# Kernel optimization log

Hardware: AMD Instinct MI355X
Metric: run time of the kernel (lower is better)

Reference implementation:

```python
import jax, jax.numpy as jnp
import numpy as np

D_K = 64
D_V = 64


def _scan_stream(q, k, v):
    """Process one stream of L tokens; q,k: (L, d_k), v: (L, d_v).
    Faithful to the torch module: update() calls update_correlations(k, q, v),
    i.e. arguments swapped, so Sigma_qv is EMA of k outer v and Sigma_qq is EMA of k outer k.
    Returns per-token cost values, shape (L,).
    """
    d_k, d_v = q.shape[-1], v.shape[-1]

    def step(carry, qkv):
        Svv, Skv, Skk, J, l = carry
        qt, kt, vt = qkv
        l = l + 1.0
        w = 1.0 / l          # omega_i
        wf = 1.0 - w         # omega_f == (l-1)/l
        Svv = wf * Svv + w * jnp.outer(vt, vt)   # (d_v, d_v)
        Skv = wf * Skv + w * jnp.outer(kt, vt)   # (d_k, d_v)  <- 'Sigma_qv' with swapped args
        Skk = wf * Skk + w * jnp.outer(kt, kt)   # (d_k, d_k)  <- 'Sigma_qq' with swapped args
        J = wf * J + w * jnp.outer(vt, kt)       # (d_v, d_k)
        # C = 1/2 Tr(Svv) - Tr(J Skv) + 1/2 Tr(J Skk J^T)
        term1 = 0.5 * jnp.trace(Svv)
        term2 = -jnp.sum(J * Skv.T)              # Tr(J @ Skv)
        term3 = 0.5 * jnp.sum((J @ Skk) * J)     # Tr(J @ Skk @ J^T)
        return (Svv, Skv, Skk, J, l), term1 + term2 + term3

    init = (jnp.zeros((d_v, d_v), q.dtype),
            jnp.zeros((d_k, d_v), q.dtype),
            jnp.zeros((d_k, d_k), q.dtype),
            jnp.zeros((d_v, d_k), q.dtype),
            jnp.asarray(0.0, q.dtype))
    _, costs = jax.lax.scan(step, init, (q, k, v))
    return costs


def setup_inputs() -> dict:
    key = jax.random.key(0)
    kq, kk, kv = jax.random.split(key, 3)
    B, L = 8, 2048
    q = jax.random.normal(kq, (B, L, D_K), dtype=jnp.float32)
    k = jax.random.normal(kk, (B, L, D_K), dtype=jnp.float32)
    v = jax.random.normal(kv, (B, L, D_V), dtype=jnp.float32)
    return {"q": q, "k": k, "v": v}


def reference(q, k, v):
    # (B, L) per-token costs for B independent memory streams
    return jax.vmap(_scan_stream)(q, k, v)
```

## Files before the change

### kernel.cpp

```cpp
#include <hip/hip_runtime.h>

#define BB 8
#define LL 2048
#define CC 64
#define NCH 32
#define SB 72

typedef float f32x4 __attribute__((ext_vector_type(4)));
typedef short bf8 __attribute__((ext_vector_type(8)));

static __device__ __forceinline__ unsigned short f2b(float f) {
  unsigned u = __builtin_bit_cast(unsigned, f);
  u += 0x7fff + ((u >> 16) & 1);
  return (unsigned short)(u >> 16);
}
static __device__ __forceinline__ float b2f(unsigned short h) {
  return __builtin_bit_cast(float, ((unsigned)h) << 16);
}
#define MFMA(A, B, C) __builtin_amdgcn_mfma_f32_16x16x32_bf16(A, B, C, 0, 0, 0)


__global__ __launch_bounds__(512, 4) void k1_mfma(const float* __restrict__ k,
                                                  const float* __restrict__ v,
                                                  unsigned short* __restrict__ pref) {
  __shared__ unsigned short sKcT[64 * SB], sVcT[64 * SB];
  int s = blockIdx.x >> 5, c = blockIdx.x & 31;
  int tid = threadIdx.x;
  int tok0 = s * LL + c * CC;
  const float* kb = k + (size_t)tok0 * 64;
  const float* vb = v + (size_t)tok0 * 64;
  {
    int r = tid >> 3, cb = (tid & 7) * 8;
    f32x4 ka_ = *(const f32x4*)(kb + r * 64 + cb);
    f32x4 kb_ = *(const f32x4*)(kb + r * 64 + cb + 4);
    f32x4 va_ = *(const f32x4*)(vb + r * 64 + cb);
    f32x4 vb_ = *(const f32x4*)(vb + r * 64 + cb + 4);
    #pragma unroll
    for (int u = 0; u < 4; ++u) {
      sKcT[(cb + u) * SB + r] = f2b(ka_[u]);
      sKcT[(cb + 4 + u) * SB + r] = f2b(kb_[u]);
      sVcT[(cb + u) * SB + r] = f2b(va_[u]);
      sVcT[(cb + 4 + u) * SB + r] = f2b(vb_[u]);
    }
  }
  __syncthreads();
  int l = tid & 63, q = tid >> 6;
  int R0 = (q & 3) * 16, C0 = (q >> 2) * 32;
  int ar = R0 + (l & 15);
  int ko = (l >> 4) * 8;
#define LDA(T, ks) (*(const bf8*)&(T)[ar * SB + ko + (ks) * 32])
#define LDB(T, nt, ks) (*(const bf8*)&(T)[(C0 + 16 * (nt) + (l & 15)) * SB + ko + (ks) * 32])
  f32x4 PA[2] = {}, PK[2] = {};
  #pragma unroll
  for (int ks = 0; ks < 2; ++ks) {
    bf8 aV = LDA(sVcT, ks), aK = LDA(sKcT, ks);
    #pragma unroll
    for (int nt = 0; nt < 2; ++nt) {
      bf8 bK = LDB(sKcT, nt, ks);
      PA[nt] = MFMA(aV, bK, PA[nt]);
      PK[nt] = MFMA(aK, bK, PK[nt]);
    }
  }
  unsigned short* dst = pref + (size_t)(s * NCH + c) * 8192;
  #pragma unroll
  for (int nt = 0; nt < 2; ++nt)
    #pragma unroll
    for (int reg = 0; reg < 4; ++reg) {
      int row = R0 + (l >> 4) * 4 + reg;
      int col = C0 + 16 * nt + (l & 15);
      dst[row * 64 + col] = f2b(PA[nt][reg]);
      dst[4096 + row * 64 + col] = f2b(PK[nt][reg]);
    }
#undef LDA
#undef LDB
}

__global__ __launch_bounds__(256) void k2_prefix(unsigned short* __restrict__ pref) {
  int gid = blockIdx.x * 256 + threadIdx.x;
  int s = gid >> 13, e = gid & 8191;
  unsigned short* base = pref + (size_t)s * NCH * 8192 + e;
  unsigned short x[16], y[16];
  #pragma unroll
  for (int u = 0; u < 16; ++u) x[u] = base[(size_t)u * 8192];
  #pragma unroll
  for (int u = 0; u < 16; ++u) y[u] = base[(size_t)(16 + u) * 8192];
  float acc = 0.f;
  #pragma unroll
  for (int u = 0; u < 16; ++u) {
    float t = b2f(x[u]);
    base[(size_t)u * 8192] = f2b(acc);
    acc += t;
  }
  #pragma unroll
  for (int u = 0; u < 16; ++u) {
    float t = b2f(y[u]);
    base[(size_t)(16 + u) * 8192] = f2b(acc);
    acc += t;
  }
}

__global__ __launch_bounds__(512, 1) void k3_mfma(const float* __restrict__ k,
                                                  const float* __restrict__ v,
                                                  const unsigned short* __restrict__ pref,
                                                  float* __restrict__ uo,
                                                  float* __restrict__ wo,
                                                  float* __restrict__ nuo) {
  __shared__ unsigned short sKc[64 * SB], sVc[64 * SB], sA0[64 * SB],
                            sK0[64 * SB], sKcT[64 * SB], sVcT[64 * SB];
  __shared__ float sdK[64], sdN[64], comb[64][2][2];
  unsigned short* sP = sK0;
  unsigned short* sY = sVcT;
  int s = blockIdx.x >> 5, c = blockIdx.x & 31;
  int tid = threadIdx.x;
  int tok0 = s * LL + c * CC;
  const float* kb = k + (size_t)tok0 * 64;
  const float* vb = v + (size_t)tok0 * 64;
  const unsigned short* gA0 = pref + (size_t)(s * NCH + c) * 8192;
  const unsigned short* gK0 = gA0 + 4096;

  {
    int r = tid >> 3, cb = (tid & 7) * 8;
    f32x4 ka_ = *(const f32x4*)(kb + r * 64 + cb);
    f32x4 kb_ = *(const f32x4*)(kb + r * 64 + cb + 4);
    f32x4 va_ = *(const f32x4*)(vb + r * 64 + cb);
    f32x4 vb_ = *(const f32x4*)(vb + r * 64 + cb + 4);
    bf8 wa = *(const bf8*)&gA0[r * 64 + cb];
    bf8 wq = *(const bf8*)&gK0[r * 64 + cb];
    bf8 wk, wv;
    #pragma unroll
    for (int u = 0; u < 4; ++u) {
      wk[u] = (short)f2b(ka_[u]); wk[4 + u] = (short)f2b(kb_[u]);
      wv[u] = (short)f2b(va_[u]); wv[4 + u] = (short)f2b(vb_[u]);
    }
    *(bf8*)&sKc[r * SB + cb] = wk;
    *(bf8*)&sVc[r * SB + cb] = wv;
    *(bf8*)&sA0[r * SB + cb] = wa;
    *(bf8*)&sK0[r * SB + cb] = wq;
    #pragma unroll
    for (int u = 0; u < 8; ++u) {
      sKcT[(cb + u) * SB + r] = (unsigned short)wk[u];
      sVcT[(cb + u) * SB + r] = (unsigned short)wv[u];
    }
  }
  __syncthreads();

  int l = tid & 63, q = tid >> 6;
  int R0 = (q & 3) * 16, C0 = (q >> 2) * 32, ch = q >> 2;
  int ar = R0 + (l & 15);
  int ko = (l >> 4) * 8;
#define LDA(T, ks) (*(const bf8*)&(T)[ar * SB + ko + (ks) * 32])
#define LDB(T, nt, ks) (*(const bf8*)&(T)[(C0 + 16 * (nt) + (l & 15)) * SB + ko + (ks) * 32])

  f32x4 X[2] = {}, Y[2] = {}, M[2] = {}, N[2] = {};
  #pragma unroll
  for (int ks = 0; ks < 2; ++ks) {
    bf8 aK = LDA(sKc, ks), aV = LDA(sVc, ks);
    #pragma unroll
    for (int nt = 0; nt < 2; ++nt) {
      M[nt] = MFMA(aK, LDB(sKc, nt, ks), M[nt]);
      N[nt] = MFMA(aV, LDB(sVc, nt, ks), N[nt]);
      X[nt] = MFMA(aK, LDB(sA0, nt, ks), X[nt]);
      Y[nt] = MFMA(aK, LDB(sK0, nt, ks), Y[nt]);
    }
  }
  __syncthreads();
  #pragma unroll
  for (int nt = 0; nt < 2; ++nt)
    #pragma unroll
    for (int reg = 0; reg < 4; ++reg) {
      int row = R0 + (l >> 4) * 4 + reg;
      int col = C0 + 16 * nt + (l & 15);
      float m = M[nt][reg];
      sP[row * SB + col] = (col < row) ? f2b(m) : (unsigned short)0;
      if (col == row) { sdK[row] = m; sdN[row] = N[nt][reg]; }
    }
  __syncthreads();
  #pragma unroll
  for (int ks = 0; ks < 2; ++ks) {
    bf8 aP = LDA(sP, ks);
    #pragma unroll
    for (int nt = 0; nt < 2; ++nt) {
      X[nt] = MFMA(aP, LDB(sVcT, nt, ks), X[nt]);
      Y[nt] = MFMA(aP, LDB(sKcT, nt, ks), Y[nt]);
    }
  }
  __syncthreads();
  #pragma unroll
  for (int nt = 0; nt < 2; ++nt)
    #pragma unroll
    for (int reg = 0; reg < 4; ++reg) {
      int row = R0 + (l >> 4) * 4 + reg;
      int col = C0 + 16 * nt + (l & 15);
      sY[row * SB + col] = f2b(Y[nt][reg]);
    }
  __syncthreads();
  f32x4 Z[2] = {}, G[2] = {};
  #pragma unroll
  for (int ks = 0; ks < 2; ++ks) {
    bf8 aY = LDA(sY, ks);
    #pragma unroll
    for (int nt = 0; nt < 2; ++nt) {
      Z[nt] = MFMA(aY, LDB(sKc, nt, ks), Z[nt]);
      G[nt] = MFMA(aY, LDB(sA0, nt, ks), G[nt]);
    }
  }
  #pragma unroll
  for (int reg = 0; reg < 4; ++reg) {
    int row = R0 + (l >> 4) * 4 + reg;
    float ka = sdK[row], nv = sdN[row];
    float pu = 0.f, pw = 0.f;
    #pragma unroll
    for (int nt = 0; nt < 2; ++nt) {
      int col = C0 + 16 * nt + (l & 15);
      float x = X[nt][reg], y = Y[nt][reg], n = N[nt][reg];
      float z = Z[nt][reg], g = G[nt][reg];
      float vtl = b2f(sVc[row * SB + col]);
      float ktl = b2f(sKc[row * SB + col]);
      float zn = (col < row) ? z * n : 0.f;
      float vx = vtl * x;
      pu += 2.f * (vtl * g + zn) + x * x + 2.f * ka * vx + nv * (ktl * y);
      pw += vx;
    }
    #pragma unroll
    for (int mm = 1; mm < 16; mm <<= 1) {
      pu += __shfl_xor(pu, mm, 64);
      pw += __shfl_xor(pw, mm, 64);
    }
    if ((l & 15) == 0) { comb[row][ch][0] = pu; comb[row][ch][1] = pw; }
  }
  __syncthreads();
  if (tid < 64) {
    float ka = sdK[tid], nv = sdN[tid];
    float u = comb[tid][0][0] + comb[tid][1][0] + ka * ka * nv;
    float w = 2.f * (comb[tid][0][1] + comb[tid][1][1]) + ka * nv;
    uo[tok0 + tid] = u;
    wo[tok0 + tid] = w;
    nuo[tok0 + tid] = nv;
  }
#undef LDA
#undef LDB
}

__global__ __launch_bounds__(256) void k4_out(const float* __restrict__ u,
                                              const float* __restrict__ w,
                                              const float* __restrict__ nu,
                                              float* __restrict__ out) {
  int s = blockIdx.x;
  int tid = threadIdx.x, l = tid & 63, wv = tid >> 6;
  __shared__ float su[4], sw[4], sn[4];
  const float* us = u + s * LL;
  const float* wsp = w + s * LL;
  const float* ns = nu + s * LL;
  float pu[8], pw[8], pn[8];
  int base = tid * 8;
  {
    float ru = 0, rw = 0, rn = 0;
    #pragma unroll
    for (int e = 0; e < 8; ++e) {
      ru += us[base + e]; pu[e] = ru;
      rw += wsp[base + e]; pw[e] = rw;
      rn += ns[base + e]; pn[e] = rn;
    }
  }
  float tu = pu[7], tw = pw[7], tn = pn[7];
  float iu = tu, iw = tw, in_ = tn;
  #pragma unroll
  for (int off = 1; off < 64; off <<= 1) {
    float a = __shfl_up(iu, off, 64);
    float b = __shfl_up(iw, off, 64);
    float c2 = __shfl_up(in_, off, 64);
    if (l >= off) { iu += a; iw += b; in_ += c2; }
  }
  if (l == 63) { su[wv] = iu; sw[wv] = iw; sn[wv] = in_; }
  __syncthreads();
  float bu = 0, bw = 0, bn = 0;
  for (int i2 = 0; i2 < wv; ++i2) { bu += su[i2]; bw += sw[i2]; bn += sn[i2]; }
  float eu = bu + iu - tu, ew = bw + iw - tw, en = bn + in_ - tn;
  float* os = out + s * LL;
  #pragma unroll
  for (int e = 0; e < 8; ++e) {
    int t = base + e;
    float inv = 1.0f / (float)(t + 1);
    float U = eu + pu[e], W = ew + pw[e], S = en + pn[e];
    os[t] = inv * (0.5f * S + inv * fmaf(0.5f * inv, U, -W));
  }
}

extern "C" void kernel_launch(void* const* d_in, const int* in_sizes, int n_in,
                              void* d_out, int out_size, void* d_ws, size_t ws_size,
                              hipStream_t stream) {
  const float* k = (const float*)d_in[1];
  const float* v = (const float*)d_in[2];
  float* out = (float*)d_out;
  float* ws = (float*)d_ws;
  unsigned short* pref = (unsigned short*)ws;
  float* nu = ws + (size_t)BB * NCH * 4096;
  float* uu = nu + BB * LL;
  float* ww = uu + BB * LL;
  hipLaunchKernelGGL(k1_mfma, dim3(BB * NCH), dim3(512), 0, stream, k, v, pref);
  hipLaunchKernelGGL(k2_prefix, dim3(BB * 8192 / 256), dim3(256), 0, stream, pref);
  hipLaunchKernelGGL(k3_mfma, dim3(BB * NCH), dim3(512), 0, stream, k, v, pref, uu, ww, nu);
  hipLaunchKernelGGL(k4_out, dim3(BB), dim3(256), 0, stream, uu, ww, nu, out);
}
```

Measured before the change: 22.94 us.

## Fuse output scan into k3 via last-block atomic, swizzle transposed LDS tiles

The final per-stream prefix/output kernel is folded into k3: each block bumps an atomic counter per stream, and the last block to finish runs the scan and writes the output. This removes one kernel launch but adds a memset launch. The transposed LDS tiles now use an XOR swizzle to cut bank conflicts on the strided transpose writes. k1 stages its results through LDS so the global stores to pref are coalesced 16-byte writes. k1's launch bounds drop the min-blocks hint from 4 to 1, and the fused tail adds serialized work inside a single block per stream.

Result: slower. 34.52 us (+50.5%).

```diff
diff --git a/kernel.cpp b/kernel.cpp
--- a/kernel.cpp
+++ b/kernel.cpp
@@ -17,10 +17,13 @@
 static __device__ __forceinline__ float b2f(unsigned short h) {
   return __builtin_bit_cast(float, ((unsigned)h) << 16);
 }
+static __device__ __forceinline__ int tswz(int row, int col) {
+  return row * SB + ((((col) >> 3) ^ ((row) >> 3)) & 7) * 8 + ((col) & 7);
+}
 #define MFMA(A, B, C) __builtin_amdgcn_mfma_f32_16x16x32_bf16(A, B, C, 0, 0, 0)
 
 
-__global__ __launch_bounds__(512, 4) void k1_mfma(const float* __restrict__ k,
+__global__ __launch_bounds__(512, 1) void k1_mfma(const float* __restrict__ k,
                                                   const float* __restrict__ v,
                                                   unsigned short* __restrict__ pref) {
   __shared__ unsigned short sKcT[64 * SB], sVcT[64 * SB];
@@ -37,10 +40,10 @@
     f32x4 vb_ = *(const f32x4*)(vb + r * 64 + cb + 4);
     #pragma unroll
     for (int u = 0; u < 4; ++u) {
-      sKcT[(cb + u) * SB + r] = f2b(ka_[u]);
-      sKcT[(cb + 4 + u) * SB + r] = f2b(kb_[u]);
-      sVcT[(cb + u) * SB + r] = f2b(va_[u]);
-      sVcT[(cb + 4 + u) * SB + r] = f2b(vb_[u]);
+      sKcT[tswz(cb + u, r)] = f2b(ka_[u]);
+      sKcT[tswz(cb + 4 + u, r)] = f2b(kb_[u]);
+      sVcT[tswz(cb + u, r)] = f2b(va_[u]);
+      sVcT[tswz(cb + 4 + u, r)] = f2b(vb_[u]);
     }
   }
   __syncthreads();
@@ -48,31 +51,35 @@
   int R0 = (q & 3) * 16, C0 = (q >> 2) * 32;
   int ar = R0 + (l & 15);
   int ko = (l >> 4) * 8;
-#define LDA(T, ks) (*(const bf8*)&(T)[ar * SB + ko + (ks) * 32])
-#define LDB(T, nt, ks) (*(const bf8*)&(T)[(C0 + 16 * (nt) + (l & 15)) * SB + ko + (ks) * 32])
   f32x4 PA[2] = {}, PK[2] = {};
   #pragma unroll
   for (int ks = 0; ks < 2; ++ks) {
-    bf8 aV = LDA(sVcT, ks), aK = LDA(sKcT, ks);
-    #pragma unroll
-    for (int nt = 0; nt < 2; ++nt) {
-      bf8 bK = LDB(sKcT, nt, ks);
+    bf8 aV = *(const bf8*)&sVcT[tswz(ar, ko + ks * 32)];
+    bf8 aK = *(const bf8*)&sKcT[tswz(ar, ko + ks * 32)];
+    #pragma unroll
+    for (int nt = 0; nt < 2; ++nt) {
+      bf8 bK = *(const bf8*)&sKcT[tswz(C0 + 16 * nt + (l & 15), ko + ks * 32)];
       PA[nt] = MFMA(aV, bK, PA[nt]);
       PK[nt] = MFMA(aK, bK, PK[nt]);
     }
   }
-  unsigned short* dst = pref + (size_t)(s * NCH + c) * 8192;
+  __syncthreads();
   #pragma unroll
   for (int nt = 0; nt < 2; ++nt)
     #pragma unroll
     for (int reg = 0; reg < 4; ++reg) {
       int row = R0 + (l >> 4) * 4 + reg;
       int col = C0 + 16 * nt + (l & 15);
-      dst[row * 64 + col] = f2b(PA[nt][reg]);
-      dst[4096 + row * 64 + col] = f2b(PK[nt][reg]);
-    }
-#undef LDA
-#undef LDB
+      sKcT[row * SB + col] = f2b(PA[nt][reg]);
+      sVcT[row * SB + col] = f2b(PK[nt][reg]);
+    }
+  __syncthreads();
+  {
+    int r2 = tid >> 3, cb2 = (tid & 7) * 8;
+    unsigned short* dst = pref + (size_t)(s * NCH + c) * 8192;
+    *(bf8*)&dst[r2 * 64 + cb2] = *(const bf8*)&sKcT[r2 * SB + cb2];
+    *(bf8*)&dst[4096 + r2 * 64 + cb2] = *(const bf8*)&sVcT[r2 * SB + cb2];
+  }
 }
 
 __global__ __launch_bounds__(256) void k2_prefix(unsigned short* __restrict__ pref) {
@@ -104,10 +111,13 @@
                                                   const unsigned short* __restrict__ pref,
                                                   float* __restrict__ uo,
                                                   float* __restrict__ wo,
-                                                  float* __restrict__ nuo) {
+                                                  float* __restrict__ nuo,
+                                                  int* __restrict__ cnt,
+                                                  float* __restrict__ out) {
   __shared__ unsigned short sKc[64 * SB], sVc[64 * SB], sA0[64 * SB],
                             sK0[64 * SB], sKcT[64 * SB], sVcT[64 * SB];
   __shared__ float sdK[64], sdN[64], comb[64][2][2];
+  __shared__ int lastflag;
   unsigned short* sP = sK0;
   unsigned short* sY = sVcT;
   int s = blockIdx.x >> 5, c = blockIdx.x & 31;
@@ -138,8 +148,8 @@
     *(bf8*)&sK0[r * SB + cb] = wq;
     #pragma unroll
     for (int u = 0; u < 8; ++u) {
-      sKcT[(cb + u) * SB + r] = (unsigned short)wk[u];
-      sVcT[(cb + u) * SB + r] = (unsigned short)wv[u];
+      sKcT[tswz(cb + u, r)] = (unsigned short)wk[u];
+      sVcT[tswz(cb + u, r)] = (unsigned short)wv[u];
     }
   }
   __syncthreads();
@@ -150,6 +160,8 @@
   int ko = (l >> 4) * 8;
 #define LDA(T, ks) (*(const bf8*)&(T)[ar * SB + ko + (ks) * 32])
 #define LDB(T, nt, ks) (*(const bf8*)&(T)[(C0 + 16 * (nt) + (l & 15)) * SB + ko + (ks) * 32])
+#define LDB_SW(T, nt, ks) (*(const bf8*)&(T)[tswz(C0 + 16 * (nt) + (l & 15), ko + (ks) * 32)])
+#define LDA_SW(T, ks) (*(const bf8*)&(T)[tswz(ar, ko + (ks) * 32)])
 
   f32x4 X[2] = {}, Y[2] = {}, M[2] = {}, N[2] = {};
   #pragma unroll
@@ -180,8 +192,8 @@
     bf8 aP = LDA(sP, ks);
     #pragma unroll
     for (int nt = 0; nt < 2; ++nt) {
-      X[nt] = MFMA(aP, LDB(sVcT, nt, ks), X[nt]);
-      Y[nt] = MFMA(aP, LDB(sKcT, nt, ks), Y[nt]);
+      X[nt] = MFMA(aP, LDB_SW(sVcT, nt, ks), X[nt]);
+      Y[nt] = MFMA(aP, LDB_SW(sKcT, nt, ks), Y[nt]);
     }
   }
   __syncthreads();
@@ -239,21 +251,29 @@
   }
 #undef LDA
 #undef LDB
-}
-
-__global__ __launch_bounds__(256) void k4_out(const float* __restrict__ u,
-                                              const float* __restrict__ w,
-                                              const float* __restrict__ nu,
-                                              float* __restrict__ out) {
-  int s = blockIdx.x;
-  int tid = threadIdx.x, l = tid & 63, wv = tid >> 6;
+#undef LDB_SW
+#undef LDA_SW
+
+  __syncthreads();
+  if (tid == 0) {
+    __threadfence();
+    int old = atomicAdd(&cnt[s], 1);
+    lastflag = (old == NCH - 1) ? 1 : 0;
+  }
+  __syncthreads();
+  if (!lastflag) return;
+  __threadfence();
+
+  bool act = tid < 256;
+  int wv = tid >> 6;
   __shared__ float su[4], sw[4], sn[4];
-  const float* us = u + s * LL;
-  const float* wsp = w + s * LL;
-  const float* ns = nu + s * LL;
+  const float* us = uo + s * LL;
+  const float* wsp = wo + s * LL;
+  const float* ns = nuo + s * LL;
   float pu[8], pw[8], pn[8];
+  float tu = 0, tw = 0, tn = 0, iu = 0, iw = 0, in_ = 0;
   int base = tid * 8;
-  {
+  if (act) {
     float ru = 0, rw = 0, rn = 0;
     #pragma unroll
     for (int e = 0; e < 8; ++e) {
@@ -261,28 +281,30 @@
       rw += wsp[base + e]; pw[e] = rw;
       rn += ns[base + e]; pn[e] = rn;
     }
-  }
-  float tu = pu[7], tw = pw[7], tn = pn[7];
-  float iu = tu, iw = tw, in_ = tn;
-  #pragma unroll
-  for (int off = 1; off < 64; off <<= 1) {
-    float a = __shfl_up(iu, off, 64);
-    float b = __shfl_up(iw, off, 64);
-    float c2 = __shfl_up(in_, off, 64);
-    if (l >= off) { iu += a; iw += b; in_ += c2; }
-  }
-  if (l == 63) { su[wv] = iu; sw[wv] = iw; sn[wv] = in_; }
-  __syncthreads();
-  float bu = 0, bw = 0, bn = 0;
-  for (int i2 = 0; i2 < wv; ++i2) { bu += su[i2]; bw += sw[i2]; bn += sn[i2]; }
-  float eu = bu + iu - tu, ew = bw + iw - tw, en = bn + in_ - tn;
-  float* os = out + s * LL;
-  #pragma unroll
-  for (int e = 0; e < 8; ++e) {
-    int t = base + e;
-    float inv = 1.0f / (float)(t + 1);
-    float U = eu + pu[e], W = ew + pw[e], S = en + pn[e];
-    os[t] = inv * (0.5f * S + inv * fmaf(0.5f * inv, U, -W));
+    tu = pu[7]; tw = pw[7]; tn = pn[7];
+    iu = tu; iw = tw; in_ = tn;
+    #pragma unroll
+    for (int off = 1; off < 64; off <<= 1) {
+      float a = __shfl_up(iu, off, 64);
+      float b = __shfl_up(iw, off, 64);
+      float c2 = __shfl_up(in_, off, 64);
+      if (l >= off) { iu += a; iw += b; in_ += c2; }
+    }
+    if (l == 63) { su[wv] = iu; sw[wv] = iw; sn[wv] = in_; }
+  }
+  __syncthreads();
+  if (act) {
+    float bu = 0, bw = 0, bn = 0;
+    for (int i2 = 0; i2 < wv; ++i2) { bu += su[i2]; bw += sw[i2]; bn += sn[i2]; }
+    float eu = bu + iu - tu, ew = bw + iw - tw, en = bn + in_ - tn;
+    float* os = out + s * LL;
+    #pragma unroll
+    for (int e = 0; e < 8; ++e) {
+      int t = base + e;
+      float inv = 1.0f / (float)(t + 1);
+      float U = eu + pu[e], W = ew + pw[e], S = en + pn[e];
+      os[t] = inv * (0.5f * S + inv * fmaf(0.5f * inv, U, -W));
+    }
   }
 }
 
@@ -297,8 +319,10 @@
   float* nu = ws + (size_t)BB * NCH * 4096;
   float* uu = nu + BB * LL;
   float* ww = uu + BB * LL;
+  int* cnt = (int*)(ww + BB * LL);
+  hipMemsetAsync(cnt, 0, BB * sizeof(int), stream);
   hipLaunchKernelGGL(k1_mfma, dim3(BB * NCH), dim3(512), 0, stream, k, v, pref);
   hipLaunchKernelGGL(k2_prefix, dim3(BB * 8192 / 256), dim3(256), 0, stream, pref);
-  hipLaunchKernelGGL(k3_mfma, dim3(BB * NCH), dim3(512), 0, stream, k, v, pref, uu, ww, nu);
-  hipLaunchKernelGGL(k4_out, dim3(BB), dim3(256), 0, stream, uu, ww, nu, out);
-}
+  hipLaunchKernelGGL(k3_mfma, dim3(BB * NCH), dim3(512), 0, stream, k, v, pref,
+                     uu, ww, nu, cnt, out);
+}
```
